# Performance work log

Measured on AMD Instinct MI355X. Metric: run time of the kernel, lower is better.

The kernel has to match this reference:

```python
import jax, jax.numpy as jnp
import numpy as np

B, T, D, H = 8, 1024, 768, 12
HD = D // H  # 64

def setup_inputs() -> dict:
    key = jax.random.key(0)
    ks = jax.random.split(key, 3)
    x = jax.random.normal(ks[0], (B, T, D), dtype=jnp.float32)
    Wqkv = jax.random.normal(ks[1], (D, 3 * D), dtype=jnp.float32) * (1.0 / np.sqrt(D))
    bqkv = jnp.zeros((3 * D,), dtype=jnp.float32)
    Wproj = jax.random.normal(ks[2], (D, D), dtype=jnp.float32) * (1.0 / np.sqrt(D))
    bproj = jnp.zeros((D,), dtype=jnp.float32)
    return {"x": x, "Wqkv": Wqkv, "bqkv": bqkv, "Wproj": Wproj, "bproj": bproj}

def reference(x, Wqkv, bqkv, Wproj, bproj):
    b, t, d = x.shape
    qkv = x @ Wqkv + bqkv                      # [B,T,3D]
    q, k, v = jnp.split(qkv, 3, axis=-1)
    # [B,T,D] -> [B,H,T,hd]
    q = q.reshape(b, t, H, HD).transpose(0, 2, 1, 3)
    k = k.reshape(b, t, H, HD).transpose(0, 2, 1, 3)
    v = v.reshape(b, t, H, HD).transpose(0, 2, 1, 3)
    scale = 1.0 / np.sqrt(HD)
    att = jnp.einsum('bhqd,bhkd->bhqk', q, k) * scale  # [B,H,T,T]
    causal = jnp.tril(jnp.ones((t, t), dtype=bool))
    att = jnp.where(causal[None, None], att, jnp.float32(-jnp.inf))
    att = jax.nn.softmax(att, axis=-1)
    out = jnp.einsum('bhqk,bhkd->bhqd', att, v)        # [B,H,T,hd]
    out = out.transpose(0, 2, 1, 3).reshape(b, t, d)
    return out @ Wproj + bproj
```

## Files before the change

### kernel.cpp

```cpp
#include <hip/hip_runtime.h>

#define Bn 8
#define Tn 1024
#define Dn 768
#define Hn 12
#define HDn 64
#define D3 (3 * Dn)

typedef float f32x4 __attribute__((ext_vector_type(4)));
typedef short bf16x8 __attribute__((ext_vector_type(8)));
typedef unsigned short u16;

#define SM_SCALE 0.18033688011112042f

__device__ __forceinline__ u16 f2b(float f) {
    unsigned u = __builtin_bit_cast(unsigned, f);
    u += 0x7fffu + ((u >> 16) & 1u);
    return (u16)(u >> 16);
}

__device__ __forceinline__ unsigned cvt_pk_bf16(float lo, float hi) {
    unsigned r;
    asm("v_cvt_pk_bf16_f32 %0, %1, %2" : "=v"(r) : "v"(lo), "v"(hi));
    return r;
}

__device__ __forceinline__ void async_lds16(void* lds, const void* g) {
    __builtin_amdgcn_global_load_lds(
        (const __attribute__((address_space(1))) unsigned int*)g,
        (__attribute__((address_space(3))) unsigned int*)lds, 16, 0, 0);
}

__global__ __launch_bounds__(256)
void conv_bf16_kernel(const float* __restrict__ in, u16* __restrict__ out, int n)
{
    int i = (blockIdx.x * 256 + threadIdx.x) * 4;
    if (i >= n) return;
    float4 v = *(const float4*)&in[i];
    union { u16 u[4]; uint2 p; } r;
    r.u[0] = f2b(v.x); r.u[1] = f2b(v.y); r.u[2] = f2b(v.z); r.u[3] = f2b(v.w);
    *(uint2*)&out[i] = r.p;
}

__global__ __launch_bounds__(256)
void transpose_bf16_kernel(const float* __restrict__ W, u16* __restrict__ WT,
                           int K, int N)
{
    __shared__ float Ls[64][65];
    const int bk = blockIdx.y * 64, bn = blockIdx.x * 64;
    const int r  = threadIdx.x >> 2;
    const int c0 = (threadIdx.x & 3) * 16;
    #pragma unroll
    for (int i = 0; i < 4; ++i) {
        float4 v = *(const float4*)&W[(size_t)(bk + r) * N + bn + c0 + i * 4];
        Ls[r][c0 + i * 4 + 0] = v.x;
        Ls[r][c0 + i * 4 + 1] = v.y;
        Ls[r][c0 + i * 4 + 2] = v.z;
        Ls[r][c0 + i * 4 + 3] = v.w;
    }
    __syncthreads();
    #pragma unroll
    for (int i = 0; i < 16; ++i) {
        WT[(size_t)(bn + r) * K + bk + c0 + i] = f2b(Ls[c0 + i][r]);
    }
}

template <int MODE, int BM, int BN>
__global__ __launch_bounds__((BM / 64) * (BN / 64) * 64)
void gemm_mfma_kernel(const u16* __restrict__ A, const u16* __restrict__ BT,
                      const float* __restrict__ bias, void* __restrict__ Cout,
                      u16* __restrict__ VTout, int M, int N, int K)
{
    constexpr int WN = BN / 64;
    constexpr int T  = (BM / 64) * WN * 64;
    constexpr int ACH = BM * 4;
    constexpr int BCH = BN * 4;

    __shared__ u16 As[2][BM * 32];
    __shared__ u16 Bs[2][BN * 32];
    const int tid  = threadIdx.x;
    const int w    = tid >> 6;
    const int lane = tid & 63;
    const int li   = lane & 15;
    const int g    = lane >> 4;
    const int wm   = w / WN;
    const int wn   = w % WN;

    const int fid = blockIdx.x;
    const int wg  = (fid & 7) * ((int)gridDim.x >> 3) + (fid >> 3);
    const int nbx = N / BN;
    const int bm  = (wg / nbx) * BM;
    const int bn  = (wg % nbx) * BN;

#define GSTAGE(k0s, buf_) do {                                                 \
        _Pragma("unroll")                                                      \
        for (int i_ = 0; i_ < ACH / T; ++i_) {                                 \
            const int L_  = i_ * T + tid;                                      \
            const int rp_ = L_ >> 3;                                           \
            const int u_  = (L_ & 7) ^ (rp_ & 7);                              \
            const int row_ = rp_ * 2 + (u_ >> 2);                              \
            const int gc_  = u_ & 3;                                           \
            async_lds16(&As[buf_][(i_ * T + w * 64) * 8],                      \
                        &A[(size_t)(bm + row_) * K + (k0s) + gc_ * 8]);        \
        }                                                                      \
        _Pragma("unroll")                                                      \
        for (int i_ = 0; i_ < BCH / T; ++i_) {                                 \
            const int L_  = i_ * T + tid;                                      \
            const int rp_ = L_ >> 3;                                           \
            const int u_  = (L_ & 7) ^ (rp_ & 7);                              \
            const int row_ = rp_ * 2 + (u_ >> 2);                              \
            const int gc_  = u_ & 3;                                           \
            async_lds16(&Bs[buf_][(i_ * T + w * 64) * 8],                      \
                        &BT[(size_t)(bn + row_) * K + (k0s) + gc_ * 8]);       \
        }                                                                      \
    } while (0)

    f32x4 acc[4][4];
    #pragma unroll
    for (int i = 0; i < 4; ++i)
        #pragma unroll
        for (int j = 0; j < 4; ++j)
            acc[i][j] = (f32x4){0.f, 0.f, 0.f, 0.f};

    GSTAGE(0, 0);
    __syncthreads();

    const int nk = K / 32;
    for (int kt = 0; kt < nk; ++kt) {
        const int cur = kt & 1;
        if (kt + 1 < nk) GSTAGE((kt + 1) * 32, cur ^ 1);

        bf16x8 af[4], bfr[4];
        #pragma unroll
        for (int fm = 0; fm < 4; ++fm) {
            const int row = wm * 64 + fm * 16 + li;
            const int rp  = row >> 1;
            const int s   = (((row & 1) << 2) | g) ^ (rp & 7);
            af[fm] = *(const bf16x8*)&As[cur][rp * 64 + s * 8];
        }
        #pragma unroll
        for (int fn = 0; fn < 4; ++fn) {
            const int row = wn * 64 + fn * 16 + li;
            const int rp  = row >> 1;
            const int s   = (((row & 1) << 2) | g) ^ (rp & 7);
            bfr[fn] = *(const bf16x8*)&Bs[cur][rp * 64 + s * 8];
        }
        __builtin_amdgcn_s_setprio(1);
        #pragma unroll
        for (int fm = 0; fm < 4; ++fm)
            #pragma unroll
            for (int fn = 0; fn < 4; ++fn)
                acc[fm][fn] = __builtin_amdgcn_mfma_f32_16x16x32_bf16(
                    af[fm], bfr[fn], acc[fm][fn], 0, 0, 0);
        __builtin_amdgcn_s_setprio(0);

        __syncthreads();
    }
#undef GSTAGE

    if (MODE == 1 && bn >= 2 * Dn) {
        #pragma unroll
        for (int fm = 0; fm < 4; ++fm) {
            const int t0g = bm + wm * 64 + fm * 16 + g * 4;
            const int bb = t0g >> 10, tt = t0g & 1023;
            #pragma unroll
            for (int fn = 0; fn < 4; ++fn) {
                const int ncol = bn + wn * 64 + fn * 16 + li;
                const float bs = bias[ncol];
                const int cv = ncol - 2 * Dn;
                const int hv = cv >> 6, dv = cv & 63;
                union { u16 u[4]; uint2 p; } r;
                #pragma unroll
                for (int reg = 0; reg < 4; ++reg)
                    r.u[reg] = f2b(acc[fm][fn][reg] + bs);
                *(uint2*)&VTout[(((size_t)bb * Hn + hv) * HDn + dv) * Tn + tt] = r.p;
            }
        }
    } else {
        #pragma unroll
        for (int fm = 0; fm < 4; ++fm) {
            #pragma unroll
            for (int reg = 0; reg < 4; ++reg) {
                const size_t row = (size_t)(bm + wm * 64 + fm * 16 + g * 4 + reg);
                #pragma unroll
                for (int fn = 0; fn < 4; ++fn) {
                    const int col = bn + wn * 64 + fn * 16 + li;
                    const float v = acc[fm][fn][reg] + bias[col];
                    if (MODE == 1) ((u16*)Cout)[row * N + col] = f2b(v);
                    else           ((float*)Cout)[row * N + col] = v;
                }
            }
        }
    }
}

__global__ __launch_bounds__(256, 3)
void attn_mfma_kernel(const u16* __restrict__ qkvb, const u16* __restrict__ VT,
                      u16* __restrict__ attnb)
{
    __shared__ u16 Ks[2][64 * 64];
    __shared__ u16 Vs[2][64 * 64];
    __shared__ u16 Pb[4][32 * 64];

    const int tid  = threadIdx.x;
    const int w    = tid >> 6;
    const int lane = tid & 63;
    const int li   = lane & 15;
    const int g    = lane >> 4;

    const int fid = blockIdx.x;
    const int xcd = fid & 7, j = fid >> 3;
    const int bh  = xcd + 8 * (j % 12);
    const int qt  = 7 - (j / 12);
    const int b   = bh / 12, h = bh % 12;

    const int q0   = qt * 128;
    const int wrow = q0 + w * 32;
    const size_t rowbase = (size_t)b * Tn;
    const u16* vbase = VT + (size_t)bh * HDn * Tn;
    const u16* kbase = &qkvb[rowbase * D3 + Dn + h * HDn];

#define STAGE(kt_, buf_) do {                                                  \
        const int k0s = (kt_) * 64;                                            \
        _Pragma("unroll")                                                      \
        for (int i_ = 0; i_ < 2; ++i_) {                                       \
            const int L_   = i_ * 256 + tid;                                   \
            const int row_ = L_ >> 3;                                          \
            const int gp_  = (L_ & 7) ^ (row_ & 7);                            \
            async_lds16(&Ks[buf_][(i_ * 256 + w * 64) * 8],                    \
                        &kbase[(size_t)(k0s + row_) * D3 + gp_ * 8]);          \
            async_lds16(&Vs[buf_][(i_ * 256 + w * 64) * 8],                    \
                        &vbase[(size_t)row_ * Tn + k0s + gp_ * 8]);            \
        }                                                                      \
    } while (0)

    STAGE(0, 0);

    bf16x8 qf[2][2];
    #pragma unroll
    for (int rh = 0; rh < 2; ++rh)
        #pragma unroll
        for (int kc = 0; kc < 2; ++kc)
            qf[rh][kc] = *(const bf16x8*)&qkvb[
                (rowbase + wrow + rh * 16 + li) * D3 + h * HDn + kc * 32 + g * 8];

    f32x4 of[2][4];
    float m_run[2], l_run[2];
    #pragma unroll
    for (int rh = 0; rh < 2; ++rh) {
        #pragma unroll
        for (int nf = 0; nf < 4; ++nf) of[rh][nf] = (f32x4){0.f, 0.f, 0.f, 0.f};
        m_run[rh] = -1e30f;
        l_run[rh] = 0.f;
    }

    const int nkt   = (q0 >> 6) + 2;
    const int myend = wrow >> 6;

    __syncthreads();

    for (int kt = 0; kt < nkt; ++kt) {
        const int cur = kt & 1;
        if (kt + 1 < nkt) STAGE(kt + 1, cur ^ 1);

        if (kt <= myend) {
            const int k0 = kt * 64;
            const bool maskit = (kt == myend);

            f32x4 st[2][4];
            #pragma unroll
            for (int rh = 0; rh < 2; ++rh)
                #pragma unroll
                for (int nf = 0; nf < 4; ++nf) st[rh][nf] = (f32x4){0.f, 0.f, 0.f, 0.f};
            __builtin_amdgcn_s_setprio(1);
            #pragma unroll
            for (int kc = 0; kc < 2; ++kc)
                #pragma unroll
                for (int nf = 0; nf < 4; ++nf) {
                    const bf16x8 kf = *(const bf16x8*)&Ks[cur][
                        (nf * 16 + li) * 64 + ((kc * 32 + g * 8) ^ ((li & 7) * 8))];
                    st[0][nf] = __builtin_amdgcn_mfma_f32_16x16x32_bf16(kf, qf[0][kc], st[0][nf], 0, 0, 0);
                    st[1][nf] = __builtin_amdgcn_mfma_f32_16x16x32_bf16(kf, qf[1][kc], st[1][nf], 0, 0, 0);
                }
            __builtin_amdgcn_s_setprio(0);

            #pragma unroll
            for (int rh = 0; rh < 2; ++rh) {
                if (maskit) {
                    const int qg = wrow + rh * 16 + li;
                    #pragma unroll
                    for (int nf = 0; nf < 4; ++nf)
                        #pragma unroll
                        for (int reg = 0; reg < 4; ++reg)
                            if (k0 + nf * 16 + g * 4 + reg > qg) st[rh][nf][reg] = -1e30f;
                }

                float mt = st[rh][0][0];
                #pragma unroll
                for (int nf = 0; nf < 4; ++nf)
                    #pragma unroll
                    for (int reg = 0; reg < 4; ++reg)
                        mt = fmaxf(mt, st[rh][nf][reg]);
                mt = fmaxf(mt, __shfl_xor(mt, 16, 64));
                mt = fmaxf(mt, __shfl_xor(mt, 32, 64));
                const float mts = mt * SM_SCALE;

                const float mold = m_run[rh];
                if (!__all(mts <= mold + 8.0f)) {
                    const float mnew = fmaxf(mold, mts);
                    const float resc = exp2f(mold - mnew);
                    m_run[rh] = mnew;
                    l_run[rh] *= resc;
                    float rs[4];
                    #pragma unroll
                    for (int reg = 0; reg < 4; ++reg)
                        rs[reg] = __shfl(resc, g * 4 + reg, 64);
                    #pragma unroll
                    for (int nf = 0; nf < 4; ++nf)
                        #pragma unroll
                        for (int reg = 0; reg < 4; ++reg)
                            of[rh][nf][reg] *= rs[reg];
                }

                const float mcur = m_run[rh];
                float ls = 0.f;
                u16* pb = &Pb[w][(rh * 16 + li) * 64];
                #pragma unroll
                for (int nf = 0; nf < 4; ++nf) {
                    const float p0 = exp2f(fmaf(st[rh][nf][0], SM_SCALE, -mcur));
                    const float p1 = exp2f(fmaf(st[rh][nf][1], SM_SCALE, -mcur));
                    const float p2 = exp2f(fmaf(st[rh][nf][2], SM_SCALE, -mcur));
                    const float p3 = exp2f(fmaf(st[rh][nf][3], SM_SCALE, -mcur));
                    ls += (p0 + p1) + (p2 + p3);
                    uint2 pk;
                    pk.x = cvt_pk_bf16(p0, p1);
                    pk.y = cvt_pk_bf16(p2, p3);
                    *(uint2*)&pb[(nf * 16 + g * 4) ^ ((li & 7) << 3)] = pk;
                }
                ls += __shfl_xor(ls, 16, 64);
                ls += __shfl_xor(ls, 32, 64);
                l_run[rh] += ls;
            }

            #pragma unroll
            for (int kc = 0; kc < 2; ++kc) {
                const int pcol = (kc * 32 + g * 8) ^ ((li & 7) << 3);
                const bf16x8 pf0 = *(const bf16x8*)&Pb[w][li * 64 + pcol];
                const bf16x8 pf1 = *(const bf16x8*)&Pb[w][(16 + li) * 64 + pcol];
                __builtin_amdgcn_s_setprio(1);
                #pragma unroll
                for (int nf = 0; nf < 4; ++nf) {
                    const bf16x8 vf = *(const bf16x8*)&Vs[cur][
                        (nf * 16 + li) * 64 + ((kc * 32 + g * 8) ^ ((li & 7) * 8))];
                    of[0][nf] = __builtin_amdgcn_mfma_f32_16x16x32_bf16(pf0, vf, of[0][nf], 0, 0, 0);
                    of[1][nf] = __builtin_amdgcn_mfma_f32_16x16x32_bf16(pf1, vf, of[1][nf], 0, 0, 0);
                }
                __builtin_amdgcn_s_setprio(0);
            }
        }

        __syncthreads();
    }
#undef STAGE

    #pragma unroll
    for (int rh = 0; rh < 2; ++rh) {
        const float inv = 1.0f / l_run[rh];
        float rs[4];
        #pragma unroll
        for (int reg = 0; reg < 4; ++reg)
            rs[reg] = __shfl(inv, g * 4 + reg, 64);
        #pragma unroll
        for (int reg = 0; reg < 4; ++reg) {
            const size_t row = rowbase + wrow + rh * 16 + g * 4 + reg;
            #pragma unroll
            for (int nf = 0; nf < 4; ++nf)
                attnb[row * Dn + h * HDn + nf * 16 + li] = f2b(of[rh][nf][reg] * rs[reg]);
        }
    }
}

extern "C" void kernel_launch(void* const* d_in, const int* in_sizes, int n_in,
                              void* d_out, int out_size, void* d_ws, size_t ws_size,
                              hipStream_t stream) {
    const float* x     = (const float*)d_in[0];
    const float* Wqkv  = (const float*)d_in[1];
    const float* bqkv  = (const float*)d_in[2];
    const float* Wproj = (const float*)d_in[3];
    const float* bproj = (const float*)d_in[4];
    float* out = (float*)d_out;

    const int M = Bn * Tn;

    char* ws = (char*)d_ws;
    u16* qkvb   = (u16*)ws;  ws += (size_t)M * D3 * 2;
    u16* xb     = (u16*)ws;  ws += (size_t)M * Dn * 2;
    u16* attnb  = (u16*)ws;  ws += (size_t)M * Dn * 2;
    u16* VT     = (u16*)ws;  ws += (size_t)Bn * Hn * HDn * Tn * 2;
    u16* WqkvT  = (u16*)ws;  ws += (size_t)D3 * Dn * 2;
    u16* WprojT = (u16*)ws;

    conv_bf16_kernel<<<(M * Dn / 4 + 255) / 256, 256, 0, stream>>>(x, xb, M * Dn);
    {
        dim3 gq(D3 / 64, Dn / 64);
        transpose_bf16_kernel<<<gq, 256, 0, stream>>>(Wqkv, WqkvT, Dn, D3);
        dim3 gp(Dn / 64, Dn / 64);
        transpose_bf16_kernel<<<gp, 256, 0, stream>>>(Wproj, WprojT, Dn, Dn);
    }
    {
        const int nwg = (M / 256) * (D3 / 128);
        gemm_mfma_kernel<1, 256, 128><<<nwg, 512, 0, stream>>>(
            xb, WqkvT, bqkv, qkvb, VT, M, D3, Dn);
    }
    attn_mfma_kernel<<<768, 256, 0, stream>>>(qkvb, VT, attnb);
    {
        const int nwg = (M / 128) * (Dn / 128);
        gemm_mfma_kernel<0, 128, 128><<<nwg, 256, 0, stream>>>(
            attnb, WprojT, bproj, out, nullptr, M, Dn, Dn);
    }
}
```

Baseline: 117.0 us.

## Add BK=64 swizzled projection GEMM, merge weight transposes, widen bf16 conversion

The output projection now uses a new GEMM kernel. It stages 64-wide K tiles into double-buffered LDS with XOR swizzling and async global-to-LDS loads, remaps workgroups by XCD, and raises wave priority around the MFMA blocks. The two weight-transpose launches become one launch with a z dimension, which drops one kernel launch. The fp32-to-bf16 conversion handles 8 elements per thread with 16-byte stores. The larger LDS footprint of the new GEMM may limit occupancy.

```diff
diff --git a/kernel.cpp b/kernel.cpp
--- a/kernel.cpp
+++ b/kernel.cpp
@@ -34,18 +34,27 @@
 __global__ __launch_bounds__(256)
 void conv_bf16_kernel(const float* __restrict__ in, u16* __restrict__ out, int n)
 {
-    int i = (blockIdx.x * 256 + threadIdx.x) * 4;
+    int i = (blockIdx.x * 256 + threadIdx.x) * 8;
     if (i >= n) return;
-    float4 v = *(const float4*)&in[i];
-    union { u16 u[4]; uint2 p; } r;
-    r.u[0] = f2b(v.x); r.u[1] = f2b(v.y); r.u[2] = f2b(v.z); r.u[3] = f2b(v.w);
-    *(uint2*)&out[i] = r.p;
+    float4 v0 = *(const float4*)&in[i];
+    float4 v1 = *(const float4*)&in[i + 4];
+    union { u16 u[8]; uint4 p; } r;
+    r.u[0] = f2b(v0.x); r.u[1] = f2b(v0.y); r.u[2] = f2b(v0.z); r.u[3] = f2b(v0.w);
+    r.u[4] = f2b(v1.x); r.u[5] = f2b(v1.y); r.u[6] = f2b(v1.z); r.u[7] = f2b(v1.w);
+    *(uint4*)&out[i] = r.p;
 }
 
 __global__ __launch_bounds__(256)
-void transpose_bf16_kernel(const float* __restrict__ W, u16* __restrict__ WT,
-                           int K, int N)
+void transpose2_bf16_kernel(const float* __restrict__ Wq, u16* __restrict__ WqT,
+                            const float* __restrict__ Wp, u16* __restrict__ WpT)
 {
+    const int z = blockIdx.z;
+    if (z == 1 && blockIdx.x >= Dn / 64) return;
+    const float* W  = z ? Wp : Wq;
+    u16* WT         = z ? WpT : WqT;
+    const int N     = z ? Dn : D3;
+    const int K     = Dn;
+
     __shared__ float Ls[64][65];
     const int bk = blockIdx.y * 64, bn = blockIdx.x * 64;
     const int r  = threadIdx.x >> 2;
@@ -194,6 +203,97 @@
     }
 }
 
+__global__ __launch_bounds__(256)
+void gemm_bk64_kernel(const u16* __restrict__ A, const u16* __restrict__ BT,
+                      const float* __restrict__ bias, float* __restrict__ C,
+                      int M, int N, int K)
+{
+    __shared__ u16 As[2][128 * 64];
+    __shared__ u16 Bs[2][128 * 64];
+    const int tid  = threadIdx.x;
+    const int w    = tid >> 6;
+    const int lane = tid & 63;
+    const int li   = lane & 15;
+    const int g    = lane >> 4;
+    const int wm   = w >> 1, wn = w & 1;
+
+    const int fid = blockIdx.x;
+    const int wg  = (fid & 7) * ((int)gridDim.x >> 3) + (fid >> 3);
+    const int nbx = N / 128;
+    const int bm  = (wg / nbx) * 128;
+    const int bn  = (wg % nbx) * 128;
+
+#define GSTAGE64(k0s, buf_) do {                                               \
+        _Pragma("unroll")                                                      \
+        for (int i_ = 0; i_ < 4; ++i_) {                                       \
+            const int L_   = i_ * 256 + tid;                                   \
+            const int row_ = L_ >> 3;                                          \
+            const int gp_  = (L_ & 7) ^ (row_ & 7);                            \
+            async_lds16(&As[buf_][(i_ * 256 + w * 64) * 8],                    \
+                        &A[(size_t)(bm + row_) * K + (k0s) + gp_ * 8]);        \
+            async_lds16(&Bs[buf_][(i_ * 256 + w * 64) * 8],                    \
+                        &BT[(size_t)(bn + row_) * K + (k0s) + gp_ * 8]);       \
+        }                                                                      \
+    } while (0)
+
+    f32x4 acc[4][4];
+    #pragma unroll
+    for (int i = 0; i < 4; ++i)
+        #pragma unroll
+        for (int j = 0; j < 4; ++j)
+            acc[i][j] = (f32x4){0.f, 0.f, 0.f, 0.f};
+
+    GSTAGE64(0, 0);
+    __syncthreads();
+
+    const int nk = K / 64;
+    for (int kt = 0; kt < nk; ++kt) {
+        const int cur = kt & 1;
+        if (kt + 1 < nk) GSTAGE64((kt + 1) * 64, cur ^ 1);
+
+        #pragma unroll
+        for (int kk = 0; kk < 2; ++kk) {
+            bf16x8 af[4], bfr[4];
+            #pragma unroll
+            for (int fm = 0; fm < 4; ++fm) {
+                const int row = wm * 64 + fm * 16 + li;
+                af[fm] = *(const bf16x8*)&As[cur][
+                    row * 64 + ((kk * 32 + g * 8) ^ ((li & 7) * 8))];
+            }
+            #pragma unroll
+            for (int fn = 0; fn < 4; ++fn) {
+                const int row = wn * 64 + fn * 16 + li;
+                bfr[fn] = *(const bf16x8*)&Bs[cur][
+                    row * 64 + ((kk * 32 + g * 8) ^ ((li & 7) * 8))];
+            }
+            __builtin_amdgcn_s_setprio(1);
+            #pragma unroll
+            for (int fm = 0; fm < 4; ++fm)
+                #pragma unroll
+                for (int fn = 0; fn < 4; ++fn)
+                    acc[fm][fn] = __builtin_amdgcn_mfma_f32_16x16x32_bf16(
+                        af[fm], bfr[fn], acc[fm][fn], 0, 0, 0);
+            __builtin_amdgcn_s_setprio(0);
+        }
+
+        __syncthreads();
+    }
+#undef GSTAGE64
+
+    #pragma unroll
+    for (int fm = 0; fm < 4; ++fm) {
+        #pragma unroll
+        for (int reg = 0; reg < 4; ++reg) {
+            const size_t row = (size_t)(bm + wm * 64 + fm * 16 + g * 4 + reg);
+            #pragma unroll
+            for (int fn = 0; fn < 4; ++fn) {
+                const int col = bn + wn * 64 + fn * 16 + li;
+                C[row * N + col] = acc[fm][fn][reg] + bias[col];
+            }
+        }
+    }
+}
+
 __global__ __launch_bounds__(256, 3)
 void attn_mfma_kernel(const u16* __restrict__ qkvb, const u16* __restrict__ VT,
                       u16* __restrict__ attnb)
@@ -400,12 +500,10 @@
     u16* WqkvT  = (u16*)ws;  ws += (size_t)D3 * Dn * 2;
     u16* WprojT = (u16*)ws;
 
-    conv_bf16_kernel<<<(M * Dn / 4 + 255) / 256, 256, 0, stream>>>(x, xb, M * Dn);
+    conv_bf16_kernel<<<M * Dn / 8 / 256, 256, 0, stream>>>(x, xb, M * Dn);
     {
-        dim3 gq(D3 / 64, Dn / 64);
-        transpose_bf16_kernel<<<gq, 256, 0, stream>>>(Wqkv, WqkvT, Dn, D3);
-        dim3 gp(Dn / 64, Dn / 64);
-        transpose_bf16_kernel<<<gp, 256, 0, stream>>>(Wproj, WprojT, Dn, Dn);
+        dim3 g(D3 / 64, Dn / 64, 2);
+        transpose2_bf16_kernel<<<g, 256, 0, stream>>>(Wqkv, WqkvT, Wproj, WprojT);
     }
     {
         const int nwg = (M / 256) * (D3 / 128);
@@ -415,7 +513,7 @@
     attn_mfma_kernel<<<768, 256, 0, stream>>>(qkvb, VT, attnb);
     {
         const int nwg = (M / 128) * (Dn / 128);
-        gemm_mfma_kernel<0, 128, 128><<<nwg, 256, 0, stream>>>(
-            attnb, WprojT, bproj, out, nullptr, M, Dn, Dn);
-    }
-}
+        gemm_bk64_kernel<<<nwg, 256, 0, stream>>>(
+            attnb, WprojT, bproj, out, M, Dn, Dn);
+    }
+}
```

New measurement: 114.4 us. 2.2% less time.
